# Optimization experiments

Hardware: AMD Instinct MI355X
Metric: run time of the kernel (lower is better)

The kernel has to match this reference:

```python
import jax, jax.numpy as jnp
import numpy as np

N = 50000      # nodes
E = 800000     # edges (avg degree 16)
IN, H, OUT = 256, 128, 64
L = 3          # num SAGEConv layers


def setup_inputs() -> dict:
    key = jax.random.key(0)
    ks = jax.random.split(key, 9)
    x = jax.random.normal(ks[0], (N, IN), dtype=jnp.float32)
    edge_index = jax.random.randint(ks[1], (2, E), 0, N, dtype=jnp.int64)
    s_in, s_h = 1.0 / np.sqrt(IN), 1.0 / np.sqrt(H)
    lin0_w = jax.random.normal(ks[2], (IN, H), dtype=jnp.float32) * s_in
    lin0_b = jnp.zeros((H,), dtype=jnp.float32)
    conv_wl = jax.random.normal(ks[3], (L, H, H), dtype=jnp.float32) * s_h  # applied to aggregated neighbors
    conv_bl = jnp.zeros((L, H), dtype=jnp.float32)
    conv_wr = jax.random.normal(ks[4], (L, H, H), dtype=jnp.float32) * s_h  # applied to root (self) features
    lin1_w = jax.random.normal(ks[5], (H, OUT), dtype=jnp.float32) * s_h
    lin1_b = jnp.zeros((OUT,), dtype=jnp.float32)
    return {"x": x, "edge_index": edge_index, "lin0_w": lin0_w, "lin0_b": lin0_b,
            "conv_wl": conv_wl, "conv_bl": conv_bl, "conv_wr": conv_wr,
            "lin1_w": lin1_w, "lin1_b": lin1_b}


def reference(x, edge_index, lin0_w, lin0_b, conv_wl, conv_bl, conv_wr, lin1_w, lin1_b):
    # Inference mode: dropout(p=0.5, training=False) is identity.
    src, dst = edge_index[0], edge_index[1]  # messages flow src -> dst (PyG source_to_target)
    deg = jax.ops.segment_sum(jnp.ones((E,), x.dtype), dst, num_segments=N)
    deg = jnp.maximum(deg, 1.0)[:, None]  # [N,1] avoid div-by-zero for isolated nodes

    h = jax.nn.relu(x @ lin0_w + lin0_b)  # [N,H]
    for i in range(L):
        # SAGEConv: lin_l(mean_agg(neighbors)) + lin_r(self)
        agg = jax.ops.segment_sum(h[src], dst, num_segments=N) / deg  # [N,H]
        h = jax.nn.relu(agg @ conv_wl[i] + conv_bl[i] + h @ conv_wr[i])
    return h @ lin1_w + lin1_b  # [N,OUT]
```

## Files before the change

kernel.cpp:

```cpp
#include <hip/hip_runtime.h>
#include <hip/hip_bf16.h>

#define N_NODES 50000
#define E_EDGES 800000
#define IN_F 256
#define H_F 128
#define OUT_F 64
#define L_LAYERS 3
#define NB_SCAN 49
#define LIN0_BLOCKS 784
#define COUNT_BLOCKS 3125
#define NPAD 50176

typedef __attribute__((ext_vector_type(8))) short bf16x8;
typedef __attribute__((ext_vector_type(4))) float f32x4;

static __device__ __forceinline__ float bf2f(unsigned short u) {
    return __uint_as_float(((unsigned int)u) << 16);
}
static __device__ __forceinline__ unsigned short f2bf(float f) {
    unsigned int b = __float_as_uint(f);
    return (unsigned short)((b + 0x7FFFu + ((b >> 16) & 1u)) >> 16);
}

__global__ __launch_bounds__(1024) void scanA_kernel(const int* __restrict__ cnt,
                                                     int* __restrict__ tmp,
                                                     int* __restrict__ bsum) {
    __shared__ int buf[1024];
    const int tid = threadIdx.x;
    const int i = blockIdx.x * 1024 + tid;
    int v = (i < N_NODES) ? cnt[(size_t)i << 4] : 0;
    buf[tid] = v;
    __syncthreads();
    for (int off = 1; off < 1024; off <<= 1) {
        int t = (tid >= off) ? buf[tid - off] : 0;
        __syncthreads();
        buf[tid] += t;
        __syncthreads();
    }
    tmp[i] = buf[tid];
    if (tid == 1023) bsum[blockIdx.x] = buf[1023];
}

__global__ void scanB_kernel(int* __restrict__ bsum) {
    int t = threadIdx.x;
    int v = (t < NB_SCAN) ? bsum[t] : 0;
    int incl = v;
    for (int off = 1; off < 64; off <<= 1) {
        int u = __shfl_up(incl, off, 64);
        if (t >= off) incl += u;
    }
    if (t < NB_SCAN) bsum[t] = incl - v;
}

__global__ __launch_bounds__(1024) void scanC_kernel(const int* __restrict__ tmp,
                                                     const int* __restrict__ bsum,
                                                     int* __restrict__ row_ptr) {
    const int i = blockIdx.x * 1024 + threadIdx.x;
    if (i < N_NODES) row_ptr[i + 1] = tmp[i] + bsum[i >> 10];
    if (i == 0) row_ptr[0] = 0;
}

__global__ void place2_kernel(const int* __restrict__ ei, const int* __restrict__ row_ptr,
                              const int* __restrict__ rank, int* __restrict__ esrc) {
    int e = blockIdx.x * blockDim.x + threadIdx.x;
    if (e < E_EDGES) {
        int s = ei[e];
        int d = ei[E_EDGES + e];
        esrc[row_ptr[d] + rank[e]] = s;
    }
}

__global__ void prep_all(const float* __restrict__ lin0_w, const float* __restrict__ conv_wl,
                         const float* __restrict__ conv_wr, const float* __restrict__ lin1_w,
                         unsigned short* __restrict__ BpL0, unsigned short* __restrict__ BpCv,
                         unsigned short* __restrict__ BpL1) {
    int gid = blockIdx.x * 256 + threadIdx.x;
    if (gid < 32768) {
        int idx = gid;
        int j = idx & 7, rest = idx >> 3;
        int c = rest & 127, gg = rest >> 7;
        BpL0[idx] = f2bf(lin0_w[(size_t)(gg * 8 + j) * 128 + c]);
    } else if (gid < 32768 + 3 * 32768) {
        int t = gid - 32768;
        int l = t >> 15, idx = t & 32767;
        int j = idx & 7, rest = idx >> 3;
        int c = rest & 127, gg = rest >> 7;
        int k = gg * 8 + j;
        const float* wl = conv_wl + (size_t)l * 16384;
        const float* wr = conv_wr + (size_t)l * 16384;
        float v = (k < 128) ? wl[(size_t)k * 128 + c] : wr[(size_t)(k - 128) * 128 + c];
        BpCv[t] = f2bf(v);
    } else if (gid < 32768 + 3 * 32768 + 8192) {
        int idx = gid - (32768 + 3 * 32768);
        int j = idx & 7, rest = idx >> 3;
        int c = rest & 63, gg = rest >> 6;
        BpL1[idx] = f2bf(lin1_w[(size_t)(gg * 8 + j) * 64 + c]);
    }
}

__global__ __launch_bounds__(256, 4) void lin0_count(
        const float* __restrict__ x, const unsigned short* __restrict__ Bp,
        const float* __restrict__ bias, unsigned short* __restrict__ hb,
        const int* __restrict__ ei, int* __restrict__ cnt, int* __restrict__ rank) {
    if (blockIdx.x >= LIN0_BLOCKS) {
        int e = (blockIdx.x - LIN0_BLOCKS) * 256 + threadIdx.x;
        if (e < E_EDGES) {
            int d = ei[E_EDGES + e];
            rank[e] = atomicAdd(&cnt[(size_t)d << 4], 1);
        }
        return;
    }
    const int tid = threadIdx.x;
    const int wave = tid >> 6, lane = tid & 63;
    const int g = lane >> 4, r = lane & 15;
    const int row_base = blockIdx.x * 64 + wave * 16;
    f32x4 acc[8] = {};
    for (int kb = 0; kb < 8; ++kb) {
        int row = min(row_base + r, N_NODES - 1);
        const float* ap = x + (size_t)row * IN_F + kb * 32 + g * 8;
        float4 v0 = *(const float4*)ap;
        float4 v1 = *(const float4*)(ap + 4);
        bf16x8 afr;
        afr[0] = (short)f2bf(v0.x); afr[1] = (short)f2bf(v0.y);
        afr[2] = (short)f2bf(v0.z); afr[3] = (short)f2bf(v0.w);
        afr[4] = (short)f2bf(v1.x); afr[5] = (short)f2bf(v1.y);
        afr[6] = (short)f2bf(v1.z); afr[7] = (short)f2bf(v1.w);
#pragma unroll
        for (int ct = 0; ct < 8; ++ct) {
            bf16x8 bfr = *(const bf16x8*)(Bp + ((size_t)((kb * 4 + g) * H_F) + ct * 16 + r) * 8);
            acc[ct] = __builtin_amdgcn_mfma_f32_16x16x32_bf16(afr, bfr, acc[ct], 0, 0, 0);
        }
    }
#pragma unroll
    for (int ct = 0; ct < 8; ++ct) {
        int col = ct * 16 + r;
        float bv = bias[col];
#pragma unroll
        for (int i = 0; i < 4; ++i) {
            int row = row_base + g * 4 + i;
            if (row < N_NODES)
                hb[(size_t)row * H_F + col] = f2bf(fmaxf(acc[ct][i] + bv, 0.f));
        }
    }
}

__global__ __launch_bounds__(256, 4) void conv_fused(
        const unsigned short* __restrict__ hb, const int* __restrict__ row_ptr,
        const int* __restrict__ esrc, const unsigned short* __restrict__ Bp,
        const float* __restrict__ bias, unsigned short* __restrict__ hbout) {
    __shared__ unsigned short sAgg[64 * 128];
    const int tid = threadIdx.x;
    const int wave = tid >> 6, lane = tid & 63;
    const int row0 = blockIdx.x * 64;

    {
        const int p = lane >> 4;
        const int q = lane & 15;
        for (int i = 0; i < 16; ++i) {
            const int ln = wave * 16 + i;
            const int node = row0 + ln;
            int s0 = 0, s1 = 0;
            if (node < N_NODES) { s0 = row_ptr[node]; s1 = row_ptr[node + 1]; }
            float a[8] = {};
            int j = s0;
            for (; j + 8 <= s1; j += 8) {
                int ea = esrc[j + p];
                int eb = esrc[j + p + 4];
                bf16x8 va = *(const bf16x8*)(hb + ((size_t)ea << 7) + (q << 3));
                bf16x8 vb = *(const bf16x8*)(hb + ((size_t)eb << 7) + (q << 3));
#pragma unroll
                for (int t = 0; t < 8; ++t)
                    a[t] += bf2f((unsigned short)va[t]) + bf2f((unsigned short)vb[t]);
            }
            if (j + p < s1) {
                bf16x8 v = *(const bf16x8*)(hb + ((size_t)esrc[j + p] << 7) + (q << 3));
#pragma unroll
                for (int t = 0; t < 8; ++t) a[t] += bf2f((unsigned short)v[t]);
            }
            if (j + p + 4 < s1) {
                bf16x8 v = *(const bf16x8*)(hb + ((size_t)esrc[j + p + 4] << 7) + (q << 3));
#pragma unroll
                for (int t = 0; t < 8; ++t) a[t] += bf2f((unsigned short)v[t]);
            }
#pragma unroll
            for (int t = 0; t < 8; ++t) {
                a[t] += __shfl_xor(a[t], 16, 64);
                a[t] += __shfl_xor(a[t], 32, 64);
            }
            if (p == 0) {
                float dinv = 1.0f / (float)max(s1 - s0, 1);
                bf16x8 o;
#pragma unroll
                for (int t = 0; t < 8; ++t) o[t] = (short)f2bf(a[t] * dinv);
                int c16 = q ^ (ln & 7);
                *(bf16x8*)(sAgg + ln * 128 + (c16 << 3)) = o;
            }
        }
    }
    __syncthreads();

    const int g = lane >> 4, r = lane & 15;
    const int row_base = row0 + wave * 16;
    f32x4 acc[8] = {};
    for (int kb = 0; kb < 8; ++kb) {
        bf16x8 afr;
        if (kb < 4) {
            int c16 = (kb * 4 + g) ^ (r & 7);
            afr = *(const bf16x8*)(sAgg + (wave * 16 + r) * 128 + (c16 << 3));
        } else {
            int row = min(row_base + r, N_NODES - 1);
            afr = *(const bf16x8*)(hb + (size_t)row * H_F + (kb & 3) * 32 + g * 8);
        }
#pragma unroll
        for (int ct = 0; ct < 8; ++ct) {
            bf16x8 bfr = *(const bf16x8*)(Bp + ((size_t)((kb * 4 + g) * H_F) + ct * 16 + r) * 8);
            acc[ct] = __builtin_amdgcn_mfma_f32_16x16x32_bf16(afr, bfr, acc[ct], 0, 0, 0);
        }
    }
#pragma unroll
    for (int ct = 0; ct < 8; ++ct) {
        int col = ct * 16 + r;
        float bv = bias[col];
#pragma unroll
        for (int i = 0; i < 4; ++i) {
            int row = row_base + g * 4 + i;
            if (row < N_NODES)
                hbout[(size_t)row * H_F + col] = f2bf(fmaxf(acc[ct][i] + bv, 0.f));
        }
    }
}

__global__ __launch_bounds__(256, 4) void lin1_mfma(
        const unsigned short* __restrict__ hb, const unsigned short* __restrict__ Bp,
        const float* __restrict__ bias, float* __restrict__ out) {
    const int tid = threadIdx.x;
    const int wave = tid >> 6, lane = tid & 63;
    const int g = lane >> 4, r = lane & 15;
    const int row_base = blockIdx.x * 64 + wave * 16;
    f32x4 acc[4] = {};
    for (int kb = 0; kb < 4; ++kb) {
        int row = min(row_base + r, N_NODES - 1);
        bf16x8 afr = *(const bf16x8*)(hb + (size_t)row * H_F + kb * 32 + g * 8);
#pragma unroll
        for (int ct = 0; ct < 4; ++ct) {
            bf16x8 bfr = *(const bf16x8*)(Bp + ((size_t)((kb * 4 + g) * OUT_F) + ct * 16 + r) * 8);
            acc[ct] = __builtin_amdgcn_mfma_f32_16x16x32_bf16(afr, bfr, acc[ct], 0, 0, 0);
        }
    }
#pragma unroll
    for (int ct = 0; ct < 4; ++ct) {
        int col = ct * 16 + r;
        float bv = bias[col];
#pragma unroll
        for (int i = 0; i < 4; ++i) {
            int row = row_base + g * 4 + i;
            if (row < N_NODES)
                out[(size_t)row * OUT_F + col] = acc[ct][i] + bv;
        }
    }
}

extern "C" void kernel_launch(void* const* d_in, const int* in_sizes, int n_in,
                              void* d_out, int out_size, void* d_ws, size_t ws_size,
                              hipStream_t stream) {
    const float* x       = (const float*)d_in[0];
    const int*   ei      = (const int*)d_in[1];
    const float* lin0_w  = (const float*)d_in[2];
    const float* lin0_b  = (const float*)d_in[3];
    const float* conv_wl = (const float*)d_in[4];
    const float* conv_bl = (const float*)d_in[5];
    const float* conv_wr = (const float*)d_in[6];
    const float* lin1_w  = (const float*)d_in[7];
    const float* lin1_b  = (const float*)d_in[8];
    float* out = (float*)d_out;

    char* ws = (char*)d_ws;
    size_t off = 0;
    auto alloc = [&](size_t bytes) {
        void* p = ws + off;
        off = (off + bytes + 255) & ~(size_t)255;
        return p;
    };
    int* cnt     = (int*)alloc((size_t)N_NODES * 16 * 4);
    int* row_ptr = (int*)alloc((size_t)(N_NODES + 1) * 4);
    int* esrc    = (int*)alloc((size_t)E_EDGES * 4);
    int* rank    = (int*)alloc((size_t)E_EDGES * 4);
    int* tmp     = (int*)alloc((size_t)NB_SCAN * 1024 * 4);
    int* bsum    = (int*)alloc(64 * 4);
    unsigned short* hb0  = (unsigned short*)alloc((size_t)NPAD * H_F * 2);
    unsigned short* hb1  = (unsigned short*)alloc((size_t)NPAD * H_F * 2);
    unsigned short* BpL0 = (unsigned short*)alloc((size_t)IN_F * H_F * 2);
    unsigned short* BpCv = (unsigned short*)alloc((size_t)L_LAYERS * 256 * H_F * 2);
    unsigned short* BpL1 = (unsigned short*)alloc((size_t)H_F * OUT_F * 2);

    hipMemsetAsync(cnt, 0, (size_t)N_NODES * 16 * 4, stream);
    prep_all<<<544, 256, 0, stream>>>(lin0_w, conv_wl, conv_wr, lin1_w, BpL0, BpCv, BpL1);

    lin0_count<<<LIN0_BLOCKS + COUNT_BLOCKS, 256, 0, stream>>>(
        x, BpL0, lin0_b, hb0, ei, cnt, rank);

    scanA_kernel<<<NB_SCAN, 1024, 0, stream>>>(cnt, tmp, bsum);
    scanB_kernel<<<1, 64, 0, stream>>>(bsum);
    scanC_kernel<<<NB_SCAN, 1024, 0, stream>>>(tmp, bsum, row_ptr);
    place2_kernel<<<COUNT_BLOCKS, 256, 0, stream>>>(ei, row_ptr, rank, esrc);

    unsigned short* h = hb0;
    unsigned short* nh = hb1;
    for (int l = 0; l < L_LAYERS; ++l) {
        conv_fused<<<NPAD / 64, 256, 0, stream>>>(h, row_ptr, esrc,
                                                  BpCv + (size_t)l * 256 * H_F,
                                                  conv_bl + (size_t)l * H_F, nh);
        unsigned short* t = h; h = nh; nh = t;
    }

    lin1_mfma<<<NPAD / 64, 256, 0, stream>>>(h, BpL1, lin1_b, out);
}
```

Measured before the change: 360.3 us.

## Halve conv block rows, split GEMM columns across waves, prefetch A rows

conv_fused now handles 32 nodes per block instead of 64 and launches twice as many blocks. The four waves split the GEMM as 2 row tiles by 2 column halves, and the gather loop gains a 16-edge unrolled step to keep more loads in flight. lin0 and lin1 preload all A-row data into registers before the MFMA loop, and the edge-count blocks are placed before the lin0 blocks in the combined launch. The aim is more parallelism and memory-level overlap in the gather-bound conv layers, at the cost of more blocks, more registers and each block reading its own copy of the weights.

```diff
diff --git a/kernel.cpp b/kernel.cpp
--- a/kernel.cpp
+++ b/kernel.cpp
@@ -99,36 +99,39 @@
     }
 }
 
-__global__ __launch_bounds__(256, 4) void lin0_count(
+__global__ __launch_bounds__(256, 3) void lin0_count(
         const float* __restrict__ x, const unsigned short* __restrict__ Bp,
         const float* __restrict__ bias, unsigned short* __restrict__ hb,
         const int* __restrict__ ei, int* __restrict__ cnt, int* __restrict__ rank) {
-    if (blockIdx.x >= LIN0_BLOCKS) {
-        int e = (blockIdx.x - LIN0_BLOCKS) * 256 + threadIdx.x;
+    if (blockIdx.x < COUNT_BLOCKS) {
+        int e = blockIdx.x * 256 + threadIdx.x;
         if (e < E_EDGES) {
             int d = ei[E_EDGES + e];
             rank[e] = atomicAdd(&cnt[(size_t)d << 4], 1);
         }
         return;
     }
+    const int gb = blockIdx.x - COUNT_BLOCKS;
     const int tid = threadIdx.x;
     const int wave = tid >> 6, lane = tid & 63;
     const int g = lane >> 4, r = lane & 15;
-    const int row_base = blockIdx.x * 64 + wave * 16;
+    const int row_base = gb * 64 + wave * 16;
+    const int row = min(row_base + r, N_NODES - 1);
+    const float* xp = x + (size_t)row * IN_F + g * 8;
+    float4 xv[16];
+#pragma unroll
+    for (int t = 0; t < 16; ++t)
+        xv[t] = *(const float4*)(xp + (t >> 1) * 32 + (t & 1) * 4);
     f32x4 acc[8] = {};
+#pragma unroll
     for (int kb = 0; kb < 8; ++kb) {
-        int row = min(row_base + r, N_NODES - 1);
-        const float* ap = x + (size_t)row * IN_F + kb * 32 + g * 8;
-        float4 v0 = *(const float4*)ap;
-        float4 v1 = *(const float4*)(ap + 4);
+        const float* v0 = (const float*)&xv[kb * 2];
         bf16x8 afr;
-        afr[0] = (short)f2bf(v0.x); afr[1] = (short)f2bf(v0.y);
-        afr[2] = (short)f2bf(v0.z); afr[3] = (short)f2bf(v0.w);
-        afr[4] = (short)f2bf(v1.x); afr[5] = (short)f2bf(v1.y);
-        afr[6] = (short)f2bf(v1.z); afr[7] = (short)f2bf(v1.w);
+#pragma unroll
+        for (int t = 0; t < 8; ++t) afr[t] = (short)f2bf(v0[t]);
 #pragma unroll
         for (int ct = 0; ct < 8; ++ct) {
-            bf16x8 bfr = *(const bf16x8*)(Bp + ((size_t)((kb * 4 + g) * H_F) + ct * 16 + r) * 8);
+            bf16x8 bfr = *(const bf16x8*)(Bp + ((size_t)(kb * 4 + g) * H_F + ct * 16 + r) * 8);
             acc[ct] = __builtin_amdgcn_mfma_f32_16x16x32_bf16(afr, bfr, acc[ct], 0, 0, 0);
         }
     }
@@ -138,9 +141,9 @@
         float bv = bias[col];
 #pragma unroll
         for (int i = 0; i < 4; ++i) {
-            int row = row_base + g * 4 + i;
-            if (row < N_NODES)
-                hb[(size_t)row * H_F + col] = f2bf(fmaxf(acc[ct][i] + bv, 0.f));
+            int orow = row_base + g * 4 + i;
+            if (orow < N_NODES)
+                hb[(size_t)orow * H_F + col] = f2bf(fmaxf(acc[ct][i] + bv, 0.f));
         }
     }
 }
@@ -149,24 +152,35 @@
         const unsigned short* __restrict__ hb, const int* __restrict__ row_ptr,
         const int* __restrict__ esrc, const unsigned short* __restrict__ Bp,
         const float* __restrict__ bias, unsigned short* __restrict__ hbout) {
-    __shared__ unsigned short sAgg[64 * 128];
+    __shared__ unsigned short sAgg[32 * 128];
     const int tid = threadIdx.x;
     const int wave = tid >> 6, lane = tid & 63;
-    const int row0 = blockIdx.x * 64;
+    const int row0 = blockIdx.x * 32;
 
     {
         const int p = lane >> 4;
         const int q = lane & 15;
-        for (int i = 0; i < 16; ++i) {
-            const int ln = wave * 16 + i;
+        for (int i = 0; i < 8; ++i) {
+            const int ln = wave * 8 + i;
             const int node = row0 + ln;
             int s0 = 0, s1 = 0;
             if (node < N_NODES) { s0 = row_ptr[node]; s1 = row_ptr[node + 1]; }
             float a[8] = {};
             int j = s0;
+            for (; j + 16 <= s1; j += 16) {
+                int ea = esrc[j + p], eb = esrc[j + p + 4];
+                int ec = esrc[j + p + 8], ed = esrc[j + p + 12];
+                bf16x8 va = *(const bf16x8*)(hb + ((size_t)ea << 7) + (q << 3));
+                bf16x8 vb = *(const bf16x8*)(hb + ((size_t)eb << 7) + (q << 3));
+                bf16x8 vc = *(const bf16x8*)(hb + ((size_t)ec << 7) + (q << 3));
+                bf16x8 vd = *(const bf16x8*)(hb + ((size_t)ed << 7) + (q << 3));
+#pragma unroll
+                for (int t = 0; t < 8; ++t)
+                    a[t] += (bf2f((unsigned short)va[t]) + bf2f((unsigned short)vb[t])) +
+                            (bf2f((unsigned short)vc[t]) + bf2f((unsigned short)vd[t]));
+            }
             for (; j + 8 <= s1; j += 8) {
-                int ea = esrc[j + p];
-                int eb = esrc[j + p + 4];
+                int ea = esrc[j + p], eb = esrc[j + p + 4];
                 bf16x8 va = *(const bf16x8*)(hb + ((size_t)ea << 7) + (q << 3));
                 bf16x8 vb = *(const bf16x8*)(hb + ((size_t)eb << 7) + (q << 3));
 #pragma unroll
@@ -201,26 +215,33 @@
     __syncthreads();
 
     const int g = lane >> 4, r = lane & 15;
-    const int row_base = row0 + wave * 16;
-    f32x4 acc[8] = {};
+    const int rt = wave & 1, ch = wave >> 1;
+    const int row_base = row0 + rt * 16;
+    const int srow = min(row_base + r, N_NODES - 1);
+    bf16x8 sv[4];
+#pragma unroll
+    for (int kb = 0; kb < 4; ++kb)
+        sv[kb] = *(const bf16x8*)(hb + (size_t)srow * H_F + kb * 32 + g * 8);
+    f32x4 acc[4] = {};
+#pragma unroll
     for (int kb = 0; kb < 8; ++kb) {
         bf16x8 afr;
         if (kb < 4) {
             int c16 = (kb * 4 + g) ^ (r & 7);
-            afr = *(const bf16x8*)(sAgg + (wave * 16 + r) * 128 + (c16 << 3));
+            afr = *(const bf16x8*)(sAgg + (rt * 16 + r) * 128 + (c16 << 3));
         } else {
-            int row = min(row_base + r, N_NODES - 1);
-            afr = *(const bf16x8*)(hb + (size_t)row * H_F + (kb & 3) * 32 + g * 8);
-        }
-#pragma unroll
-        for (int ct = 0; ct < 8; ++ct) {
-            bf16x8 bfr = *(const bf16x8*)(Bp + ((size_t)((kb * 4 + g) * H_F) + ct * 16 + r) * 8);
+            afr = sv[kb - 4];
+        }
+#pragma unroll
+        for (int ct = 0; ct < 4; ++ct) {
+            int col = ch * 64 + ct * 16 + r;
+            bf16x8 bfr = *(const bf16x8*)(Bp + ((size_t)(kb * 4 + g) * H_F + col) * 8);
             acc[ct] = __builtin_amdgcn_mfma_f32_16x16x32_bf16(afr, bfr, acc[ct], 0, 0, 0);
         }
     }
 #pragma unroll
-    for (int ct = 0; ct < 8; ++ct) {
-        int col = ct * 16 + r;
+    for (int ct = 0; ct < 4; ++ct) {
+        int col = ch * 64 + ct * 16 + r;
         float bv = bias[col];
 #pragma unroll
         for (int i = 0; i < 4; ++i) {
@@ -238,14 +259,18 @@
     const int wave = tid >> 6, lane = tid & 63;
     const int g = lane >> 4, r = lane & 15;
     const int row_base = blockIdx.x * 64 + wave * 16;
+    const int row = min(row_base + r, N_NODES - 1);
+    bf16x8 av[4];
+#pragma unroll
+    for (int kb = 0; kb < 4; ++kb)
+        av[kb] = *(const bf16x8*)(hb + (size_t)row * H_F + kb * 32 + g * 8);
     f32x4 acc[4] = {};
+#pragma unroll
     for (int kb = 0; kb < 4; ++kb) {
-        int row = min(row_base + r, N_NODES - 1);
-        bf16x8 afr = *(const bf16x8*)(hb + (size_t)row * H_F + kb * 32 + g * 8);
 #pragma unroll
         for (int ct = 0; ct < 4; ++ct) {
-            bf16x8 bfr = *(const bf16x8*)(Bp + ((size_t)((kb * 4 + g) * OUT_F) + ct * 16 + r) * 8);
-            acc[ct] = __builtin_amdgcn_mfma_f32_16x16x32_bf16(afr, bfr, acc[ct], 0, 0, 0);
+            bf16x8 bfr = *(const bf16x8*)(Bp + ((size_t)(kb * 4 + g) * OUT_F + ct * 16 + r) * 8);
+            acc[ct] = __builtin_amdgcn_mfma_f32_16x16x32_bf16(av[kb], bfr, acc[ct], 0, 0, 0);
         }
     }
 #pragma unroll
@@ -254,9 +279,9 @@
         float bv = bias[col];
 #pragma unroll
         for (int i = 0; i < 4; ++i) {
-            int row = row_base + g * 4 + i;
-            if (row < N_NODES)
-                out[(size_t)row * OUT_F + col] = acc[ct][i] + bv;
+            int orow = row_base + g * 4 + i;
+            if (orow < N_NODES)
+                out[(size_t)orow * OUT_F + col] = acc[ct][i] + bv;
         }
     }
 }
@@ -297,7 +322,7 @@
     hipMemsetAsync(cnt, 0, (size_t)N_NODES * 16 * 4, stream);
     prep_all<<<544, 256, 0, stream>>>(lin0_w, conv_wl, conv_wr, lin1_w, BpL0, BpCv, BpL1);
 
-    lin0_count<<<LIN0_BLOCKS + COUNT_BLOCKS, 256, 0, stream>>>(
+    lin0_count<<<COUNT_BLOCKS + LIN0_BLOCKS, 256, 0, stream>>>(
         x, BpL0, lin0_b, hb0, ei, cnt, rank);
 
     scanA_kernel<<<NB_SCAN, 1024, 0, stream>>>(cnt, tmp, bsum);
@@ -308,7 +333,7 @@
     unsigned short* h = hb0;
     unsigned short* nh = hb1;
     for (int l = 0; l < L_LAYERS; ++l) {
-        conv_fused<<<NPAD / 64, 256, 0, stream>>>(h, row_ptr, esrc,
+        conv_fused<<<NPAD / 32, 256, 0, stream>>>(h, row_ptr, esrc,
                                                   BpCv + (size_t)l * 256 * H_F,
                                                   conv_bl + (size_t)l * H_F, nh);
         unsigned short* t = h; h = nh; nh = t;
```

Result: faster. 310.8 us (-13.8%).
